# Optimization experiments

Measured on AMD Instinct MI355X. Metric: run time of the kernel, lower is better.

The kernel has to match this reference:

```python
import jax, jax.numpy as jnp
import numpy as np

EMB = 1024
HEADS = 16
DH = EMB // HEADS


def setup_inputs() -> dict:
    key = jax.random.key(0)
    ks = jax.random.split(key, 9)
    B, S = 4, 2048
    scale = 1.0 / np.sqrt(EMB)
    x = jax.random.normal(ks[0], (B, S, EMB), dtype=jnp.float32)
    Wq = jax.random.normal(ks[1], (EMB, EMB), dtype=jnp.float32) * scale
    Wk = jax.random.normal(ks[2], (EMB, EMB), dtype=jnp.float32) * scale
    Wv = jax.random.normal(ks[3], (EMB, EMB), dtype=jnp.float32) * scale
    Wo = jax.random.normal(ks[4], (EMB, EMB), dtype=jnp.float32) * scale
    bq = jnp.zeros((EMB,), jnp.float32)
    bk = jnp.zeros((EMB,), jnp.float32)
    bv = jnp.zeros((EMB,), jnp.float32)
    bo = jnp.zeros((EMB,), jnp.float32)
    return {"x": x, "Wq": Wq, "bq": bq, "Wk": Wk, "bk": bk,
            "Wv": Wv, "bv": bv, "Wo": Wo, "bo": bo}


def _split_heads(t):
    B, S, _ = t.shape
    return t.reshape(B, S, HEADS, DH).transpose(0, 2, 1, 3)  # [B,H,S,Dh]


def reference(x, Wq, bq, Wk, bk, Wv, bv, Wo, bo):
    q = _split_heads(x @ Wq + bq)
    k = _split_heads(x @ Wk + bk)
    v = _split_heads(x @ Wv + bv)
    # scaled dot-product attention, full [B,H,S,S] score matrix as in source
    logits = jnp.einsum("bhqd,bhkd->bhqk", q, k) / jnp.sqrt(jnp.float32(DH))
    attn = jax.nn.softmax(logits, axis=-1)
    ctx = jnp.einsum("bhqk,bhkd->bhqd", attn, v)
    B, _, S, _ = ctx.shape
    concat = ctx.transpose(0, 2, 1, 3).reshape(B, S, EMB)
    return concat @ Wo + bo
```

## Files before the change

### kernel.cpp

```cpp
#include <hip/hip_runtime.h>
#include <hip/hip_bf16.h>
#include <stdint.h>

typedef __bf16 bf16;
typedef __bf16 bf16x4 __attribute__((ext_vector_type(4)));
typedef __bf16 bf16x8 __attribute__((ext_vector_type(8)));
typedef float f32x4 __attribute__((ext_vector_type(4)));

__device__ __forceinline__ void async_ld16(const void* g, void* l) {
  __builtin_amdgcn_global_load_lds(
      (__attribute__((address_space(1))) void*)(void*)(g),
      (__attribute__((address_space(3))) void*)(l), 16, 0, 0);
}

__device__ __forceinline__ bf16 fast_bf16(float f) {
  uint32_t u = (__float_as_uint(f) + 0x8000u) >> 16;
  union { uint16_t s; bf16 b; } cv;
  cv.s = (uint16_t)u;
  return cv.b;
}

__device__ __forceinline__ uint32_t pack_bf16(float lo, float hi) {
  return __builtin_amdgcn_perm(__float_as_uint(hi) + 0x8000u,
                               __float_as_uint(lo) + 0x8000u, 0x07060302u);
}

__global__ __launch_bounds__(256) void cast_f32_bf16(const float* __restrict__ in,
                                                     bf16* __restrict__ out, int n) {
  int i = (blockIdx.x * 256 + threadIdx.x) * 4;
  if (i < n) {
    float4 f = *(const float4*)(in + i);
    uint2 o;
    o.x = pack_bf16(f.x, f.y);
    o.y = pack_bf16(f.z, f.w);
    *(uint2*)(out + i) = o;
  }
}

__global__ __launch_bounds__(256) void transpose_weights(const float* __restrict__ Wq,
                                                         const float* __restrict__ Wk,
                                                         const float* __restrict__ Wv,
                                                         const float* __restrict__ Wo,
                                                         bf16* __restrict__ Wt,
                                                         bf16* __restrict__ Wot) {
  __shared__ bf16 tile[64][66];
  int z = blockIdx.z;
  const float* src = z == 0 ? Wq : (z == 1 ? Wk : (z == 2 ? Wv : Wo));
  bf16* dst = z == 0 ? Wt : (z == 1 ? Wt + 1048576 : (z == 2 ? Wt + 2097152 : Wot));
  int r0 = blockIdx.x * 64, c0 = blockIdx.y * 64;
  int t = threadIdx.x;
#pragma unroll
  for (int i = 0; i < 16; ++i) {
    int idx = t + i * 256;
    int r = idx >> 6, c = idx & 63;
    tile[r][c] = fast_bf16(src[(size_t)(r0 + r) * 1024 + (c0 + c)]);
  }
  __syncthreads();
#pragma unroll
  for (int i = 0; i < 16; ++i) {
    int idx = t + i * 256;
    int c = idx >> 6, r = idx & 63;
    dst[(size_t)(c0 + c) * 1024 + (r0 + r)] = tile[r][c];
  }
}

__device__ __forceinline__ void gemm128_mainloop(const bf16* __restrict__ A,
                                                 const bf16* __restrict__ Bt, int K,
                                                 int rowBase, int colBase,
                                                 bf16* As, bf16* Bs,
                                                 f32x4 (&acc)[4][4]) {
  int t = threadIdx.x, lane = t & 63, w = t >> 6;
  int wM = w >> 1, wN = w & 1, quad = lane >> 4, l15 = lane & 15;
  int r_off = lane >> 3;
  int c_sw = (((lane & 7) ^ r_off) << 3);
  int sw = l15 & 7;
  for (int k0 = 0; k0 < K; k0 += 64) {
    __syncthreads();
#pragma unroll
    for (int i = 0; i < 4; ++i) {
      int e = i * 2048 + w * 512;
      int row = (e >> 6) + r_off;
      async_ld16(A + (size_t)(rowBase + row) * K + (k0 + c_sw), As + e);
      async_ld16(Bt + (size_t)(colBase + row) * K + (k0 + c_sw), Bs + e);
    }
    __syncthreads();
#pragma unroll
    for (int ks = 0; ks < 2; ++ks) {
      int co = (((ks * 4 + quad) ^ sw) << 3);
      bf16x8 af[4], bfr[4];
#pragma unroll
      for (int mi = 0; mi < 4; ++mi)
        af[mi] = *(const bf16x8*)(As + (wM * 64 + mi * 16 + l15) * 64 + co);
#pragma unroll
      for (int ni = 0; ni < 4; ++ni)
        bfr[ni] = *(const bf16x8*)(Bs + (wN * 64 + ni * 16 + l15) * 64 + co);
#pragma unroll
      for (int mi = 0; mi < 4; ++mi)
#pragma unroll
        for (int ni = 0; ni < 4; ++ni)
          acc[mi][ni] = __builtin_amdgcn_mfma_f32_16x16x32_bf16(af[mi], bfr[ni], acc[mi][ni], 0, 0, 0);
    }
  }
}

__global__ __launch_bounds__(256) void gemm_qkv(const bf16* __restrict__ X,
                                                const bf16* __restrict__ Wt,
                                                const float* __restrict__ bq,
                                                const float* __restrict__ bk,
                                                const float* __restrict__ bv,
                                                bf16* __restrict__ Qo,
                                                bf16* __restrict__ Ko,
                                                bf16* __restrict__ Vto) {
  __shared__ alignas(16) bf16 As[128 * 64];
  __shared__ alignas(16) bf16 Bs[128 * 64];
  f32x4 acc[4][4];
  f32x4 z = {0.f, 0.f, 0.f, 0.f};
#pragma unroll
  for (int mi = 0; mi < 4; ++mi)
#pragma unroll
    for (int ni = 0; ni < 4; ++ni) acc[mi][ni] = z;
  int rowBase = blockIdx.x * 128, colBase = blockIdx.y * 128;
  gemm128_mainloop(X, Wt, 1024, rowBase, colBase, As, Bs, acc);

  int t = threadIdx.x, lane = t & 63, w = t >> 6;
  int wM = w >> 1, wN = w & 1, quad = lane >> 4, l15 = lane & 15;
  int which = colBase >> 10;

  if (which == 2) {
#pragma unroll
    for (int mi = 0; mi < 4; ++mi)
#pragma unroll
      for (int ni = 0; ni < 4; ++ni) {
        int n = colBase + wN * 64 + ni * 16 + l15;
        int e = n & 1023;
        int h = e >> 6, d = e & 63;
        float bb = bv[e];
        int m0 = rowBase + wM * 64 + mi * 16 + quad * 4;
        int b = m0 >> 11, s = m0 & 2047;
        uint2 pv;
        pv.x = pack_bf16(acc[mi][ni][0] + bb, acc[mi][ni][1] + bb);
        pv.y = pack_bf16(acc[mi][ni][2] + bb, acc[mi][ni][3] + bb);
        *(uint2*)(Vto + (((size_t)((b << 4) + h) * 64 + d) << 11) + s) = pv;
      }
  } else {
    const float* bias = which == 0 ? bq : bk;
    bf16* dst = which == 0 ? Qo : Ko;
    float scale = which == 0 ? 0.125f * 1.44269504f : 1.0f;
#pragma unroll
    for (int mi = 0; mi < 4; ++mi)
#pragma unroll
      for (int ni = 0; ni < 4; ++ni) {
        int n = colBase + wN * 64 + ni * 16 + l15;
        int e = n & 1023;
        int h = e >> 6, d = e & 63;
        float bb = bias[e];
#pragma unroll
        for (int r = 0; r < 4; ++r) {
          int m = rowBase + wM * 64 + mi * 16 + quad * 4 + r;
          int b = m >> 11, s = m & 2047;
          dst[(((size_t)((b << 4) + h) * 2048 + s) << 6) + d] =
              fast_bf16((acc[mi][ni][r] + bb) * scale);
        }
      }
  }
}

__global__ __launch_bounds__(256) void gemm_out(const bf16* __restrict__ Cb,
                                                const bf16* __restrict__ Wot,
                                                const float* __restrict__ bo,
                                                float* __restrict__ out) {
  __shared__ alignas(16) bf16 As[128 * 64];
  __shared__ alignas(16) bf16 Bs[128 * 64];
  f32x4 acc[4][4];
  f32x4 z = {0.f, 0.f, 0.f, 0.f};
#pragma unroll
  for (int mi = 0; mi < 4; ++mi)
#pragma unroll
    for (int ni = 0; ni < 4; ++ni) acc[mi][ni] = z;
  int rowBase = blockIdx.x * 128, colBase = blockIdx.y * 128;
  gemm128_mainloop(Cb, Wot, 1024, rowBase, colBase, As, Bs, acc);

  int t = threadIdx.x, lane = t & 63, w = t >> 6;
  int wM = w >> 1, wN = w & 1, quad = lane >> 4, l15 = lane & 15;
#pragma unroll
  for (int mi = 0; mi < 4; ++mi)
#pragma unroll
    for (int ni = 0; ni < 4; ++ni) {
      int n = colBase + wN * 64 + ni * 16 + l15;
      float bb = bo[n];
#pragma unroll
      for (int r = 0; r < 4; ++r) {
        int m = rowBase + wM * 64 + mi * 16 + quad * 4 + r;
        out[(size_t)m * 1024 + n] = acc[mi][ni][r] + bb;
      }
    }
}

__global__ __launch_bounds__(256, 2) void attn(const bf16* __restrict__ Q,
                                               const bf16* __restrict__ Kg,
                                               const bf16* __restrict__ Vt,
                                               bf16* __restrict__ ctx) {
  __shared__ alignas(16) bf16 QPs[256 * 64];
  __shared__ alignas(16) bf16 Ks[2][64 * 64];
  __shared__ alignas(16) bf16 Vs[2][64 * 64];

  int t = threadIdx.x, lane = t & 63, w = t >> 6;
  int quad = lane >> 4, l15 = lane & 15;
  int r_off = lane >> 3;
  int c_sw = (((lane & 7) ^ r_off) << 3);
  int sw = l15 & 7;
  int bh = blockIdx.y;
  int q0 = blockIdx.x * 256;
  const bf16* Qp = Q + ((size_t)bh * 2048 + q0) * 64;
  const bf16* Kp = Kg + (size_t)bh * 2048 * 64;
  const bf16* Vp = Vt + (size_t)bh * 64 * 2048;

#pragma unroll
  for (int i = 0; i < 8; ++i) {
    int e = w * 4096 + i * 512;
    int row = (e >> 6) + r_off;
    async_ld16(Qp + (size_t)row * 64 + c_sw, QPs + e);
  }
#pragma unroll
  for (int i = 0; i < 2; ++i) {
    int e = w * 1024 + i * 512;
    int row = (e >> 6) + r_off;
    async_ld16(Kp + (size_t)row * 64 + c_sw, Ks[0] + e);
    async_ld16(Vp + (size_t)row * 2048 + c_sw, Vs[0] + e);
  }
  __syncthreads();

  bf16x8 qf[2][4];
#pragma unroll
  for (int ks = 0; ks < 2; ++ks)
#pragma unroll
    for (int qi = 0; qi < 4; ++qi)
      qf[ks][qi] = *(const bf16x8*)(QPs + (w * 64 + qi * 16 + l15) * 64 + (((ks * 4 + quad) ^ sw) << 3));
  asm volatile("s_waitcnt lgkmcnt(0)" ::: "memory");

  bf16* Ps = QPs + w * 4096;

  f32x4 o[4][4];
  f32x4 z = {0.f, 0.f, 0.f, 0.f};
  float lpart[4] = {0.f, 0.f, 0.f, 0.f};
#pragma unroll
  for (int mi = 0; mi < 4; ++mi)
#pragma unroll
    for (int ni = 0; ni < 4; ++ni) o[mi][ni] = z;

  for (int kt = 0; kt < 32; ++kt) {
    int cur = kt & 1;
    if (kt < 31) {
      int kn = (kt + 1) * 64;
#pragma unroll
      for (int i = 0; i < 2; ++i) {
        int e = w * 1024 + i * 512;
        int row = (e >> 6) + r_off;
        async_ld16(Kp + (size_t)(kn + row) * 64 + c_sw, Ks[cur ^ 1] + e);
        async_ld16(Vp + (size_t)row * 2048 + kn + c_sw, Vs[cur ^ 1] + e);
      }
    }

    f32x4 sc[4][4];
#pragma unroll
    for (int ki = 0; ki < 4; ++ki)
#pragma unroll
      for (int qi = 0; qi < 4; ++qi) sc[ki][qi] = z;
#pragma unroll
    for (int ks = 0; ks < 2; ++ks) {
      int co = (((ks * 4 + quad) ^ sw) << 3);
      bf16x8 kf[4];
#pragma unroll
      for (int ki = 0; ki < 4; ++ki)
        kf[ki] = *(const bf16x8*)(Ks[cur] + (ki * 16 + l15) * 64 + co);
#pragma unroll
      for (int ki = 0; ki < 4; ++ki)
#pragma unroll
        for (int qi = 0; qi < 4; ++qi)
          sc[ki][qi] = __builtin_amdgcn_mfma_f32_16x16x32_bf16(kf[ki], qf[ks][qi], sc[ki][qi], 0, 0, 0);
    }

#pragma unroll
    for (int qi = 0; qi < 4; ++qi)
#pragma unroll
      for (int ki = 0; ki < 4; ++ki) {
        float p0 = __builtin_amdgcn_exp2f(sc[ki][qi][0]);
        float p1 = __builtin_amdgcn_exp2f(sc[ki][qi][1]);
        float p2 = __builtin_amdgcn_exp2f(sc[ki][qi][2]);
        float p3 = __builtin_amdgcn_exp2f(sc[ki][qi][3]);
        lpart[qi] += (p0 + p1) + (p2 + p3);
        uint2 pb;
        pb.x = pack_bf16(p0, p1);
        pb.y = pack_bf16(p2, p3);
        int cs = (ki * 2 + (quad >> 1)) ^ sw;
        *(uint2*)(Ps + (qi * 16 + l15) * 64 + cs * 8 + (quad & 1) * 4) = pb;
      }

    asm volatile("s_waitcnt lgkmcnt(0)" ::: "memory");

#pragma unroll
    for (int ks = 0; ks < 2; ++ks) {
      int co = (((ks * 4 + quad) ^ sw) << 3);
      bf16x8 pf[4], vf[4];
#pragma unroll
      for (int mi = 0; mi < 4; ++mi)
        pf[mi] = *(const bf16x8*)(Ps + (mi * 16 + l15) * 64 + co);
#pragma unroll
      for (int ni = 0; ni < 4; ++ni)
        vf[ni] = *(const bf16x8*)(Vs[cur] + (ni * 16 + l15) * 64 + co);
#pragma unroll
      for (int mi = 0; mi < 4; ++mi)
#pragma unroll
        for (int ni = 0; ni < 4; ++ni)
          o[mi][ni] = __builtin_amdgcn_mfma_f32_16x16x32_bf16(pf[mi], vf[ni], o[mi][ni], 0, 0, 0);
    }

    __syncthreads();
  }

  int b = bh >> 4, h = bh & 15;
#pragma unroll
  for (int mi = 0; mi < 4; ++mi) {
    float l = lpart[mi];
    l += __shfl_xor(l, 16, 64);
    l += __shfl_xor(l, 32, 64);
    float rl[4];
#pragma unroll
    for (int r = 0; r < 4; ++r) rl[r] = 1.0f / __shfl(l, quad * 4 + r, 64);
#pragma unroll
    for (int ni = 0; ni < 4; ++ni) {
      int col = h * 64 + ni * 16 + l15;
#pragma unroll
      for (int r = 0; r < 4; ++r) {
        int q = q0 + w * 64 + mi * 16 + quad * 4 + r;
        ctx[(size_t)(b * 2048 + q) * 1024 + col] = fast_bf16(o[mi][ni][r] * rl[r]);
      }
    }
  }
}

extern "C" void kernel_launch(void* const* d_in, const int* in_sizes, int n_in,
                              void* d_out, int out_size, void* d_ws, size_t ws_size,
                              hipStream_t stream) {
  const float* x  = (const float*)d_in[0];
  const float* Wq = (const float*)d_in[1];
  const float* bq = (const float*)d_in[2];
  const float* Wk = (const float*)d_in[3];
  const float* bk = (const float*)d_in[4];
  const float* Wv = (const float*)d_in[5];
  const float* bv = (const float*)d_in[6];
  const float* Wo = (const float*)d_in[7];
  const float* bo = (const float*)d_in[8];
  float* out = (float*)d_out;

  char* ws = (char*)d_ws;
  const size_t MB = 1048576;
  bf16* xb  = (bf16*)(ws);
  bf16* Wt  = (bf16*)(ws + 16 * MB);
  bf16* Wot = (bf16*)(ws + 22 * MB);
  bf16* Qb  = (bf16*)(ws + 24 * MB);
  bf16* Kb  = (bf16*)(ws + 40 * MB);
  bf16* Vtb = (bf16*)(ws + 56 * MB);
  bf16* Cx  = (bf16*)(ws + 72 * MB);

  cast_f32_bf16<<<8192, 256, 0, stream>>>(x, xb, 8388608);
  transpose_weights<<<dim3(16, 16, 4), 256, 0, stream>>>(Wq, Wk, Wv, Wo, Wt, Wot);
  gemm_qkv<<<dim3(64, 24, 1), 256, 0, stream>>>(xb, Wt, bq, bk, bv, Qb, Kb, Vtb);
  attn<<<dim3(8, 64, 1), 256, 0, stream>>>(Qb, Kb, Vtb, Cx);
  gemm_out<<<dim3(64, 8, 1), 256, 0, stream>>>(Cx, Wot, bo, out);
}
```

Before: 291.2 us.

## Split attention key tile into halves, compute row sums by MFMA, stage V stores

```diff
diff --git a/kernel.cpp b/kernel.cpp
--- a/kernel.cpp
+++ b/kernel.cpp
@@ -111,8 +111,9 @@
                                                 bf16* __restrict__ Qo,
                                                 bf16* __restrict__ Ko,
                                                 bf16* __restrict__ Vto) {
-  __shared__ alignas(16) bf16 As[128 * 64];
-  __shared__ alignas(16) bf16 Bs[128 * 64];
+  __shared__ alignas(16) bf16 smem[2 * 128 * 64];
+  bf16* As = smem;
+  bf16* Bs = smem + 128 * 64;
   f32x4 acc[4][4];
   f32x4 z = {0.f, 0.f, 0.f, 0.f};
 #pragma unroll
@@ -127,21 +128,35 @@
   int which = colBase >> 10;
 
   if (which == 2) {
-#pragma unroll
-    for (int mi = 0; mi < 4; ++mi)
-#pragma unroll
-      for (int ni = 0; ni < 4; ++ni) {
-        int n = colBase + wN * 64 + ni * 16 + l15;
-        int e = n & 1023;
-        int h = e >> 6, d = e & 63;
-        float bb = bv[e];
-        int m0 = rowBase + wM * 64 + mi * 16 + quad * 4;
-        int b = m0 >> 11, s = m0 & 2047;
-        uint2 pv;
-        pv.x = pack_bf16(acc[mi][ni][0] + bb, acc[mi][ni][1] + bb);
-        pv.y = pack_bf16(acc[mi][ni][2] + bb, acc[mi][ni][3] + bb);
-        *(uint2*)(Vto + (((size_t)((b << 4) + h) * 64 + d) << 11) + s) = pv;
-      }
+    int baseh = (colBase & 1023) >> 6;
+    int b = rowBase >> 11, s0 = rowBase & 2047;
+#pragma unroll
+    for (int hp = 0; hp < 2; ++hp) {
+      __syncthreads();
+      if (wN == hp) {
+#pragma unroll
+        for (int mi = 0; mi < 4; ++mi)
+#pragma unroll
+          for (int ni = 0; ni < 4; ++ni) {
+            int d = ni * 16 + l15;
+            float bb = bv[(colBase & 1023) + hp * 64 + d];
+            int sl = wM * 64 + mi * 16 + quad * 4;
+            uint2 pv;
+            pv.x = pack_bf16(acc[mi][ni][0] + bb, acc[mi][ni][1] + bb);
+            pv.y = pack_bf16(acc[mi][ni][2] + bb, acc[mi][ni][3] + bb);
+            *(uint2*)(smem + d * 136 + sl) = pv;
+          }
+      }
+      __syncthreads();
+      int hg = baseh + hp;
+#pragma unroll
+      for (int it = 0; it < 4; ++it) {
+        int idx = t + it * 256;
+        int d = idx >> 4, c = idx & 15;
+        bf16x8 vv = *(const bf16x8*)(smem + d * 136 + c * 8);
+        *(bf16x8*)(Vto + (((size_t)((b << 4) + hg) << 6) + d) * 2048 + s0 + c * 8) = vv;
+      }
+    }
   } else {
     const float* bias = which == 0 ? bq : bk;
     bf16* dst = which == 0 ? Qo : Ko;
@@ -200,9 +215,8 @@
                                                const bf16* __restrict__ Kg,
                                                const bf16* __restrict__ Vt,
                                                bf16* __restrict__ ctx) {
-  __shared__ alignas(16) bf16 QPs[256 * 64];
-  __shared__ alignas(16) bf16 Ks[2][64 * 64];
-  __shared__ alignas(16) bf16 Vs[2][64 * 64];
+  __shared__ alignas(16) bf16 KVs[4][4096];
+  __shared__ alignas(16) bf16 Ps[4][2048];
 
   int t = threadIdx.x, lane = t & 63, w = t >> 6;
   int quad = lane >> 4, l15 = lane & 15;
@@ -217,116 +231,166 @@
 
 #pragma unroll
   for (int i = 0; i < 8; ++i) {
-    int e = w * 4096 + i * 512;
-    int row = (e >> 6) + r_off;
-    async_ld16(Qp + (size_t)row * 64 + c_sw, QPs + e);
-  }
+    int e = i * 512;
+    int row = i * 8 + r_off;
+    async_ld16(Qp + (size_t)(w * 64 + row) * 64 + c_sw, KVs[w] + e);
+  }
+  __syncthreads();
+
+  bf16x8 qf[2][4];
+#pragma unroll
+  for (int ks = 0; ks < 2; ++ks)
+#pragma unroll
+    for (int qi = 0; qi < 4; ++qi)
+      qf[ks][qi] = *(const bf16x8*)(KVs[w] + (qi * 16 + l15) * 64 + (((ks * 4 + quad) ^ sw) << 3));
+  __syncthreads();
+
 #pragma unroll
   for (int i = 0; i < 2; ++i) {
     int e = w * 1024 + i * 512;
     int row = (e >> 6) + r_off;
-    async_ld16(Kp + (size_t)row * 64 + c_sw, Ks[0] + e);
-    async_ld16(Vp + (size_t)row * 2048 + c_sw, Vs[0] + e);
-  }
-  __syncthreads();
-
-  bf16x8 qf[2][4];
-#pragma unroll
-  for (int ks = 0; ks < 2; ++ks)
-#pragma unroll
-    for (int qi = 0; qi < 4; ++qi)
-      qf[ks][qi] = *(const bf16x8*)(QPs + (w * 64 + qi * 16 + l15) * 64 + (((ks * 4 + quad) ^ sw) << 3));
-  asm volatile("s_waitcnt lgkmcnt(0)" ::: "memory");
-
-  bf16* Ps = QPs + w * 4096;
+    async_ld16(Kp + (size_t)row * 64 + c_sw, KVs[0] + e);
+    async_ld16(Vp + (size_t)row * 2048 + c_sw, KVs[2] + e);
+  }
+
+  bf16 one1 = (bf16)1.0f;
+  bf16x8 ones = {one1, one1, one1, one1, one1, one1, one1, one1};
+  bf16* Pw = Ps[w];
 
   f32x4 o[4][4];
+  f32x4 ol[4];
   f32x4 z = {0.f, 0.f, 0.f, 0.f};
-  float lpart[4] = {0.f, 0.f, 0.f, 0.f};
-#pragma unroll
-  for (int mi = 0; mi < 4; ++mi)
+#pragma unroll
+  for (int mi = 0; mi < 4; ++mi) {
+    ol[mi] = z;
 #pragma unroll
     for (int ni = 0; ni < 4; ++ni) o[mi][ni] = z;
+  }
 
   for (int kt = 0; kt < 32; ++kt) {
     int cur = kt & 1;
+    __syncthreads();
     if (kt < 31) {
       int kn = (kt + 1) * 64;
 #pragma unroll
       for (int i = 0; i < 2; ++i) {
         int e = w * 1024 + i * 512;
         int row = (e >> 6) + r_off;
-        async_ld16(Kp + (size_t)(kn + row) * 64 + c_sw, Ks[cur ^ 1] + e);
-        async_ld16(Vp + (size_t)row * 2048 + kn + c_sw, Vs[cur ^ 1] + e);
-      }
-    }
-
-    f32x4 sc[4][4];
-#pragma unroll
-    for (int ki = 0; ki < 4; ++ki)
-#pragma unroll
-      for (int qi = 0; qi < 4; ++qi) sc[ki][qi] = z;
+        async_ld16(Kp + (size_t)(kn + row) * 64 + c_sw, KVs[cur ^ 1] + e);
+        async_ld16(Vp + (size_t)row * 2048 + kn + c_sw, KVs[2 + (cur ^ 1)] + e);
+      }
+    }
+    const bf16* Kc = KVs[cur];
+    const bf16* Vc = KVs[2 + cur];
+
+    f32x4 sA[2][4];
+#pragma unroll
+    for (int ki = 0; ki < 2; ++ki)
+#pragma unroll
+      for (int qi = 0; qi < 4; ++qi) sA[ki][qi] = z;
 #pragma unroll
     for (int ks = 0; ks < 2; ++ks) {
       int co = (((ks * 4 + quad) ^ sw) << 3);
-      bf16x8 kf[4];
-#pragma unroll
-      for (int ki = 0; ki < 4; ++ki)
-        kf[ki] = *(const bf16x8*)(Ks[cur] + (ki * 16 + l15) * 64 + co);
-#pragma unroll
-      for (int ki = 0; ki < 4; ++ki)
-#pragma unroll
-        for (int qi = 0; qi < 4; ++qi)
-          sc[ki][qi] = __builtin_amdgcn_mfma_f32_16x16x32_bf16(kf[ki], qf[ks][qi], sc[ki][qi], 0, 0, 0);
-    }
-
+      bf16x8 kf0 = *(const bf16x8*)(Kc + (l15)*64 + co);
+      bf16x8 kf1 = *(const bf16x8*)(Kc + (16 + l15) * 64 + co);
+#pragma unroll
+      for (int qi = 0; qi < 4; ++qi) {
+        sA[0][qi] = __builtin_amdgcn_mfma_f32_16x16x32_bf16(kf0, qf[ks][qi], sA[0][qi], 0, 0, 0);
+        sA[1][qi] = __builtin_amdgcn_mfma_f32_16x16x32_bf16(kf1, qf[ks][qi], sA[1][qi], 0, 0, 0);
+      }
+    }
 #pragma unroll
     for (int qi = 0; qi < 4; ++qi)
 #pragma unroll
-      for (int ki = 0; ki < 4; ++ki) {
-        float p0 = __builtin_amdgcn_exp2f(sc[ki][qi][0]);
-        float p1 = __builtin_amdgcn_exp2f(sc[ki][qi][1]);
-        float p2 = __builtin_amdgcn_exp2f(sc[ki][qi][2]);
-        float p3 = __builtin_amdgcn_exp2f(sc[ki][qi][3]);
-        lpart[qi] += (p0 + p1) + (p2 + p3);
+      for (int ki = 0; ki < 2; ++ki) {
+        float p0 = __builtin_amdgcn_exp2f(sA[ki][qi][0]);
+        float p1 = __builtin_amdgcn_exp2f(sA[ki][qi][1]);
+        float p2 = __builtin_amdgcn_exp2f(sA[ki][qi][2]);
+        float p3 = __builtin_amdgcn_exp2f(sA[ki][qi][3]);
         uint2 pb;
         pb.x = pack_bf16(p0, p1);
         pb.y = pack_bf16(p2, p3);
-        int cs = (ki * 2 + (quad >> 1)) ^ sw;
-        *(uint2*)(Ps + (qi * 16 + l15) * 64 + cs * 8 + (quad & 1) * 4) = pb;
-      }
-
-    asm volatile("s_waitcnt lgkmcnt(0)" ::: "memory");
-
+        *(uint2*)(Pw + (qi * 16 + l15) * 32 + ki * 16 + quad * 4) = pb;
+      }
+
+    f32x4 sB[2][4];
+#pragma unroll
+    for (int ki = 0; ki < 2; ++ki)
+#pragma unroll
+      for (int qi = 0; qi < 4; ++qi) sB[ki][qi] = z;
 #pragma unroll
     for (int ks = 0; ks < 2; ++ks) {
       int co = (((ks * 4 + quad) ^ sw) << 3);
+      bf16x8 kf2 = *(const bf16x8*)(Kc + (32 + l15) * 64 + co);
+      bf16x8 kf3 = *(const bf16x8*)(Kc + (48 + l15) * 64 + co);
+#pragma unroll
+      for (int qi = 0; qi < 4; ++qi) {
+        sB[0][qi] = __builtin_amdgcn_mfma_f32_16x16x32_bf16(kf2, qf[ks][qi], sB[0][qi], 0, 0, 0);
+        sB[1][qi] = __builtin_amdgcn_mfma_f32_16x16x32_bf16(kf3, qf[ks][qi], sB[1][qi], 0, 0, 0);
+      }
+    }
+
+    asm volatile("s_waitcnt lgkmcnt(0)" ::: "memory");
+
+    {
+      int co = ((quad ^ sw) << 3);
       bf16x8 pf[4], vf[4];
 #pragma unroll
       for (int mi = 0; mi < 4; ++mi)
-        pf[mi] = *(const bf16x8*)(Ps + (mi * 16 + l15) * 64 + co);
+        pf[mi] = *(const bf16x8*)(Pw + (mi * 16 + l15) * 32 + quad * 8);
 #pragma unroll
       for (int ni = 0; ni < 4; ++ni)
-        vf[ni] = *(const bf16x8*)(Vs[cur] + (ni * 16 + l15) * 64 + co);
-#pragma unroll
-      for (int mi = 0; mi < 4; ++mi)
+        vf[ni] = *(const bf16x8*)(Vc + (ni * 16 + l15) * 64 + co);
+#pragma unroll
+      for (int mi = 0; mi < 4; ++mi) {
 #pragma unroll
         for (int ni = 0; ni < 4; ++ni)
           o[mi][ni] = __builtin_amdgcn_mfma_f32_16x16x32_bf16(pf[mi], vf[ni], o[mi][ni], 0, 0, 0);
-    }
-
-    __syncthreads();
+        ol[mi] = __builtin_amdgcn_mfma_f32_16x16x32_bf16(pf[mi], ones, ol[mi], 0, 0, 0);
+      }
+    }
+
+#pragma unroll
+    for (int qi = 0; qi < 4; ++qi)
+#pragma unroll
+      for (int ki = 0; ki < 2; ++ki) {
+        float p0 = __builtin_amdgcn_exp2f(sB[ki][qi][0]);
+        float p1 = __builtin_amdgcn_exp2f(sB[ki][qi][1]);
+        float p2 = __builtin_amdgcn_exp2f(sB[ki][qi][2]);
+        float p3 = __builtin_amdgcn_exp2f(sB[ki][qi][3]);
+        uint2 pb;
+        pb.x = pack_bf16(p0, p1);
+        pb.y = pack_bf16(p2, p3);
+        *(uint2*)(Pw + (qi * 16 + l15) * 32 + ki * 16 + quad * 4) = pb;
+      }
+
+    asm volatile("s_waitcnt lgkmcnt(0)" ::: "memory");
+
+    {
+      int co = (((4 + quad) ^ sw) << 3);
+      bf16x8 pf[4], vf[4];
+#pragma unroll
+      for (int mi = 0; mi < 4; ++mi)
+        pf[mi] = *(const bf16x8*)(Pw + (mi * 16 + l15) * 32 + quad * 8);
+#pragma unroll
+      for (int ni = 0; ni < 4; ++ni)
+        vf[ni] = *(const bf16x8*)(Vc + (ni * 16 + l15) * 64 + co);
+#pragma unroll
+      for (int mi = 0; mi < 4; ++mi) {
+#pragma unroll
+        for (int ni = 0; ni < 4; ++ni)
+          o[mi][ni] = __builtin_amdgcn_mfma_f32_16x16x32_bf16(pf[mi], vf[ni], o[mi][ni], 0, 0, 0);
+        ol[mi] = __builtin_amdgcn_mfma_f32_16x16x32_bf16(pf[mi], ones, ol[mi], 0, 0, 0);
+      }
+    }
   }
 
   int b = bh >> 4, h = bh & 15;
 #pragma unroll
   for (int mi = 0; mi < 4; ++mi) {
-    float l = lpart[mi];
-    l += __shfl_xor(l, 16, 64);
-    l += __shfl_xor(l, 32, 64);
     float rl[4];
 #pragma unroll
-    for (int r = 0; r < 4; ++r) rl[r] = 1.0f / __shfl(l, quad * 4 + r, 64);
+    for (int r = 0; r < 4; ++r) rl[r] = 1.0f / ol[mi][r];
 #pragma unroll
     for (int ni = 0; ni < 4; ++ni) {
       int col = h * 64 + ni * 16 + l15;
```

Measured after the change: 310.7 us. +6.7%, slower.
